# Kernel optimization log

Measured on AMD Instinct MI355X. Metric: run time of the kernel, lower is better.

## Reference

```python
import jax, jax.numpy as jnp
import numpy as np

B, S, D = 4, 2048, 1024
NEG = -1e9

def setup_inputs() -> dict:
    key = jax.random.key(0)
    ks = jax.random.split(key, 12)
    sc = 1.0 / np.sqrt(D)
    inp = {
        'query': jax.random.normal(ks[0], (B, S, D), jnp.float32),
        'key':   jax.random.normal(ks[1], (B, S, D), jnp.float32),
        'value': jax.random.normal(ks[2], (B, S, D), jnp.float32),
        'Wq': jax.random.normal(ks[3], (D, D), jnp.float32) * sc,
        'bq': jnp.zeros((D,), jnp.float32),
        'Wk': jax.random.normal(ks[4], (D, D), jnp.float32) * sc,
        'bk': jnp.zeros((D,), jnp.float32),
        'Wv': jax.random.normal(ks[5], (D, D), jnp.float32) * sc,
        'bv': jnp.zeros((D,), jnp.float32),
        'Wo': jax.random.normal(ks[6], (D, D), jnp.float32) * sc,
        'bo': jnp.zeros((D,), jnp.float32),
    }
    return inp

def reference(query, key, value, Wq, bq, Wk, bk, Wv, bv, Wo, bo):
    d_model = query.shape[-1]
    q = query @ Wq + bq            # [B,S,D]
    k = key   @ Wk + bk
    v = value @ Wv + bv
    # scores scaled by sqrt(d_model) (single head, full d_model)
    scores = jnp.einsum('bqd,bkd->bqk', q, k) / jnp.sqrt(jnp.float32(d_model))
    s = scores.shape[-1]
    causal = jnp.tril(jnp.ones((s, s), bool))  # True = keep
    scores = jnp.where(causal, scores, NEG)
    # log-softmax then exp for numerical stability (use_log_probs=True)
    attn = jnp.exp(jax.nn.log_softmax(scores, axis=-1))
    out = jnp.einsum('bqk,bkd->bqd', attn, v)
    return out @ Wo + bo
```

## Files before the change

kernel.cpp:

```cpp
#include <hip/hip_runtime.h>


typedef __attribute__((ext_vector_type(8))) short bf16x8_t;
typedef __attribute__((ext_vector_type(4))) float f32x4_t;

static __device__ __forceinline__ unsigned short f2b(float f) {
  union { float f; unsigned u; } c; c.f = f;
  unsigned u = c.u;
  u += 0x7fffu + ((u >> 16) & 1u);
  return (unsigned short)(u >> 16);
}

static __device__ __forceinline__ void gload16(const void* g, const void* l) {
  __builtin_amdgcn_global_load_lds(
      (const __attribute__((address_space(1))) void*)g,
      (__attribute__((address_space(3))) void*)(void*)(unsigned short*)l,
      16, 0, 0);
}

__global__ __launch_bounds__(256)
void prep_all(const float* __restrict__ q, const float* __restrict__ k,
              const float* __restrict__ v,
              unsigned short* __restrict__ qin, unsigned short* __restrict__ kin,
              unsigned short* __restrict__ vin,
              const float* __restrict__ wq, const float* __restrict__ wk,
              const float* __restrict__ wo, const float* __restrict__ wv,
              unsigned short* __restrict__ oq, unsigned short* __restrict__ ok,
              unsigned short* __restrict__ oo, unsigned short* __restrict__ ov)
{
  __shared__ unsigned short t[32][34];
  const int d = blockIdx.x;
  const int tid = threadIdx.x;
  if (d < 12288) {
    const int z = d >> 12;
    const int blk = d & 4095;
    const float* in = z == 0 ? q : (z == 1 ? k : v);
    unsigned short* out = z == 0 ? qin : (z == 1 ? kin : vin);
    const size_t base = ((size_t)blk * 256 + tid) * 8;
    const float4 x0 = *(const float4*)(in + base);
    const float4 x1 = *(const float4*)(in + base + 4);
    union { unsigned u[4]; uint4 v4; } pk;
    pk.u[0] = f2b(x0.x) | ((unsigned)f2b(x0.y) << 16);
    pk.u[1] = f2b(x0.z) | ((unsigned)f2b(x0.w) << 16);
    pk.u[2] = f2b(x1.x) | ((unsigned)f2b(x1.y) << 16);
    pk.u[3] = f2b(x1.z) | ((unsigned)f2b(x1.w) << 16);
    *(uint4*)(out + base) = pk.v4;
    return;
  }
  const int tt = d - 12288;
  const int z = tt >> 10;
  const int r = tt & 1023;
  const int by = r >> 5, bx = r & 31;
  const int x = tid & 31, y = tid >> 5;
  const float* in = z == 0 ? wq : (z == 1 ? wk : (z == 2 ? wo : wv));
  unsigned short* out = z == 0 ? oq : (z == 1 ? ok : (z == 2 ? oo : ov));
  if (z == 3) {
#pragma unroll
    for (int yy = y; yy < 32; yy += 8) {
      const int rr = by * 32 + yy, cc = bx * 32 + x;
      out[(size_t)rr * 1024 + cc] = f2b(in[(size_t)rr * 1024 + cc]);
    }
    return;
  }
#pragma unroll
  for (int yy = y; yy < 32; yy += 8)
    t[yy][x] = f2b(in[(size_t)(by * 32 + yy) * 1024 + bx * 32 + x]);
  __syncthreads();
#pragma unroll
  for (int yy = y; yy < 32; yy += 8)
    out[(size_t)(bx * 32 + yy) * 1024 + by * 32 + x] = t[x][yy];
}

template<bool OUT_BF16, int MODE>
static __device__ __forceinline__
void gemm_body(const unsigned short* __restrict__ Ab,
               const unsigned short* __restrict__ Bt,
               const float* __restrict__ bias, void* __restrict__ Cp,
               float* __restrict__ rowsum,
               int kEnd, int lda, int ldb, int ldc, float scale, int bx, int by)
{
  __shared__ unsigned short As[128 * 64];
  __shared__ unsigned short Bs[128 * 64];

  const int tid  = threadIdx.x;
  const int lane = tid & 63;
  const int wid  = tid >> 6;
  const int wr   = wid >> 1, wc = wid & 1;
  const int l15  = lane & 15, l4 = lane >> 4;

  const int srow_l = lane >> 3;
  const int schk   = lane & 7;

  f32x4_t acc[4][4];
#pragma unroll
  for (int m = 0; m < 4; ++m)
#pragma unroll
    for (int n = 0; n < 4; ++n) acc[m][n] = (f32x4_t){0.f, 0.f, 0.f, 0.f};

  for (int k0 = 0; k0 < kEnd; k0 += 64) {
#pragma unroll
    for (int i = 0; i < 4; ++i) {
      const int row = i * 32 + wid * 8 + srow_l;
      const size_t gr = (size_t)(by * 128 + row);
      const int g = schk ^ (row & 7);
      gload16(Ab + gr * lda + k0 + g * 8, &As[(i * 32 + wid * 8) * 64]);
    }
#pragma unroll
    for (int i = 0; i < 4; ++i) {
      const int row = i * 32 + wid * 8 + srow_l;
      const size_t gn = (size_t)(bx * 128 + row);
      const int g = schk ^ (row & 7);
      gload16(Bt + gn * ldb + k0 + g * 8, &Bs[(i * 32 + wid * 8) * 64]);
    }
    __syncthreads();

#pragma unroll
    for (int kk = 0; kk < 2; ++kk) {
      bf16x8_t a[4], b[4];
#pragma unroll
      for (int m = 0; m < 4; ++m) {
        const int row = wr * 64 + m * 16 + l15;
        const int c = (kk * 4 + l4) ^ (row & 7);
        a[m] = *(const bf16x8_t*)&As[row * 64 + c * 8];
      }
#pragma unroll
      for (int n = 0; n < 4; ++n) {
        const int row = wc * 64 + n * 16 + l15;
        const int c = (kk * 4 + l4) ^ (row & 7);
        b[n] = *(const bf16x8_t*)&Bs[row * 64 + c * 8];
      }
#pragma unroll
      for (int m = 0; m < 4; ++m)
#pragma unroll
        for (int n = 0; n < 4; ++n)
          acc[m][n] = __builtin_amdgcn_mfma_f32_16x16x32_bf16(a[m], b[n], acc[m][n], 0, 0, 0);
    }
    __syncthreads();
  }

  float*          Cf = (float*)Cp;
  unsigned short* Cb = (unsigned short*)Cp;
  if constexpr (MODE == 1) {
#pragma unroll
    for (int m = 0; m < 4; ++m)
#pragma unroll
      for (int j = 0; j < 4; ++j) {
        const int row = by * 128 + wr * 64 + m * 16 + l4 * 4 + j;
        float rsum = 0.f;
#pragma unroll
        for (int n = 0; n < 4; ++n) {
          const int col = bx * 128 + wc * 64 + n * 16 + l15;
          const float e = (col <= row) ? __expf(acc[m][n][j] * scale) : 0.f;
          Cb[(size_t)row * ldc + col] = f2b(e);
          rsum += e;
        }
#pragma unroll
        for (int off = 1; off < 16; off <<= 1) rsum += __shfl_xor(rsum, off);
        if (l15 == 0) atomicAdd(&rowsum[row], rsum);
      }
  } else if constexpr (MODE == 2) {
#pragma unroll
    for (int m = 0; m < 4; ++m)
#pragma unroll
      for (int n = 0; n < 4; ++n) {
        const int col = bx * 128 + wc * 64 + n * 16 + l15;
        const float bv = bias[col];
#pragma unroll
        for (int j = 0; j < 4; ++j) {
          const int row = by * 128 + wr * 64 + m * 16 + l4 * 4 + j;
          const float inv = 1.0f / rowsum[row];
          Cf[(size_t)row * ldc + col] = acc[m][n][j] * inv + bv;
        }
      }
  } else {
#pragma unroll
    for (int m = 0; m < 4; ++m)
#pragma unroll
      for (int n = 0; n < 4; ++n) {
        const int col = bx * 128 + wc * 64 + n * 16 + l15;
        const float bv = bias ? bias[col] : 0.f;
#pragma unroll
        for (int j = 0; j < 4; ++j) {
          const int row = by * 128 + wr * 64 + m * 16 + l4 * 4 + j;
          const float val = acc[m][n][j] * scale + bv;
          if (OUT_BF16) Cb[(size_t)row * ldc + col] = f2b(val);
          else          Cf[(size_t)row * ldc + col] = val;
        }
      }
  }
}

__global__ __launch_bounds__(256)
void wvo_bias2(const unsigned short* __restrict__ Wot,
               const unsigned short* __restrict__ Wvb,
               const float* __restrict__ bv, const float* __restrict__ Wo,
               const float* __restrict__ bo,
               unsigned short* __restrict__ WvoT_w, float* __restrict__ bias2)
{
  if (blockIdx.x < 64) {
    gemm_body<true, 0>(Wot, Wvb, nullptr, WvoT_w, nullptr,
                       1024, 1024, 1024, 1024, 1.f,
                       (int)blockIdx.x & 7, (int)blockIdx.x >> 3);
    return;
  }
  __shared__ float red[16][17];
  const int b = blockIdx.x - 64;
  const int ci = threadIdx.x & 15;
  const int rg = threadIdx.x >> 4;
  const int col = b * 16 + ci;
  float s = 0.f;
#pragma unroll 4
  for (int r = rg; r < 1024; r += 16)
    s += bv[r] * Wo[(size_t)r * 1024 + col];
  red[rg][ci] = s;
  __syncthreads();
  if (rg == 0) {
    float t = 0.f;
#pragma unroll
    for (int i = 0; i < 16; ++i) t += red[i][ci];
    bias2[col] = t + bo[col];
  }
}

__global__ __launch_bounds__(256)
void gemm_qkv3(const unsigned short* __restrict__ qin,
               const unsigned short* __restrict__ kin,
               const unsigned short* __restrict__ vin,
               const unsigned short* __restrict__ Wqt,
               const unsigned short* __restrict__ Wkt,
               const unsigned short* __restrict__ WvoT_w,
               const float* __restrict__ bq, const float* __restrict__ bk,
               unsigned short* __restrict__ qbuf, unsigned short* __restrict__ kbuf,
               unsigned short* __restrict__ vT)
{
  const int d = blockIdx.x;
  const int xcd = d & 7, j = d >> 3;
  const int G = xcd * 24 + (j >> 3);
  if (G < 64) {
    gemm_body<true, 0>(qin, Wqt, bq, qbuf, nullptr,
                       1024, 1024, 1024, 1024, 1.f, j & 7, G);
  } else if (G < 128) {
    gemm_body<true, 0>(kin, Wkt, bk, kbuf, nullptr,
                       1024, 1024, 1024, 1024, 1.f, j & 7, G - 64);
  } else {
    const int idx = (G - 128) * 8 + (j & 7);
    const int b  = idx >> 7;
    const int r  = idx & 127;
    const int by = r >> 4;
    const int bx = r & 15;
    gemm_body<true, 0>(WvoT_w, vin + (size_t)b * 2048 * 1024, nullptr,
                       vT + (size_t)b * 1024 * 2048, nullptr,
                       1024, 1024, 1024, 2048, 1.f, bx, by);
  }
}

__global__ __launch_bounds__(256)
void gemm_scores(const unsigned short* __restrict__ Q,
                 const unsigned short* __restrict__ Kb,
                 unsigned short* __restrict__ P, float* __restrict__ rowsum)
{
  const int d = blockIdx.x;
  const int t = (d & 7) * 68 + (d >> 3);
  const int bz = t / 136;
  const int tri = t - bz * 136;
  int by = (int)((sqrtf(8.f * tri + 1.f) - 1.f) * 0.5f);
  while ((by + 1) * (by + 2) / 2 <= tri) ++by;
  while (by * (by + 1) / 2 > tri) --by;
  const int bx = tri - by * (by + 1) / 2;
  gemm_body<true, 1>(Q + (size_t)bz * 2048 * 1024,
                     Kb + (size_t)bz * 2048 * 1024, nullptr,
                     P + (size_t)bz * 2048 * 2048,
                     rowsum + (size_t)bz * 2048,
                     1024, 1024, 1024, 2048, 0.03125f, bx, by);
}

__global__ __launch_bounds__(256)
void gemm_final(const unsigned short* __restrict__ P,
                const unsigned short* __restrict__ vT,
                const float* __restrict__ bias2, float* __restrict__ rowsum,
                float* __restrict__ out)
{
  const int d = blockIdx.x;
  const int xcd = d & 7, j = d >> 3;
  const int G = xcd * 8 + (j >> 3);
  const int bz = G >> 4;
  const int by = G & 15;
  const int bx = j & 7;
  const int kEnd = (by + 1) * 128;
  gemm_body<false, 2>(P + (size_t)bz * 2048 * 2048,
                      vT + (size_t)bz * 1024 * 2048, bias2,
                      out + (size_t)bz * 2048 * 1024,
                      rowsum + (size_t)bz * 2048,
                      kEnd, 2048, 2048, 1024, 1.f, bx, by);
}

extern "C" void kernel_launch(void* const* d_in, const int* in_sizes, int n_in,
                              void* d_out, int out_size, void* d_ws, size_t ws_size,
                              hipStream_t stream)
{
  const float* query = (const float*)d_in[0];
  const float* key   = (const float*)d_in[1];
  const float* value = (const float*)d_in[2];
  const float* Wq    = (const float*)d_in[3];
  const float* bq    = (const float*)d_in[4];
  const float* Wk    = (const float*)d_in[5];
  const float* bk    = (const float*)d_in[6];
  const float* Wv    = (const float*)d_in[7];
  const float* bv    = (const float*)d_in[8];
  const float* Wo    = (const float*)d_in[9];
  const float* bo    = (const float*)d_in[10];
  float* out = (float*)d_out;

  char* ws = (char*)d_ws;
  const size_t MB = 1024 * 1024;
  unsigned short* Wqt    = (unsigned short*)(ws + 0 * MB);
  unsigned short* Wkt    = (unsigned short*)(ws + 2 * MB);
  unsigned short* Wot    = (unsigned short*)(ws + 4 * MB);
  unsigned short* Wvb    = (unsigned short*)(ws + 6 * MB);
  unsigned short* WvoT_w = (unsigned short*)(ws + 8 * MB);
  float*          bias2  = (float*)(ws + 10 * MB);
  float*          rowsum = (float*)(ws + 11 * MB);
  unsigned short* qbuf   = (unsigned short*)(ws + 12 * MB);
  unsigned short* kbuf   = (unsigned short*)(ws + 28 * MB);
  unsigned short* vT     = (unsigned short*)(ws + 44 * MB);
  unsigned short* qin    = (unsigned short*)(ws + 60 * MB);
  unsigned short* kin    = (unsigned short*)(ws + 76 * MB);
  unsigned short* vin    = (unsigned short*)(ws + 92 * MB);
  unsigned short* Pbuf   = (unsigned short*)(ws + 108 * MB);

  hipMemsetAsync(rowsum, 0, 4 * 2048 * sizeof(float), stream);

  prep_all<<<16384, 256, 0, stream>>>(query, key, value, qin, kin, vin,
                                      Wq, Wk, Wo, Wv, Wqt, Wkt, Wot, Wvb);

  wvo_bias2<<<128, 256, 0, stream>>>(Wot, Wvb, bv, Wo, bo, WvoT_w, bias2);

  gemm_qkv3<<<1536, 256, 0, stream>>>(qin, kin, vin, Wqt, Wkt, WvoT_w,
                                      bq, bk, qbuf, kbuf, vT);

  gemm_scores<<<544, 256, 0, stream>>>(qbuf, kbuf, Pbuf, rowsum);

  gemm_final<<<512, 256, 0, stream>>>(Pbuf, vT, bias2, rowsum, out);
}
```

Measured before the change: 332.3 us.

## Regroup GEMM stages to merge Wvo product with QK projections and vT with scores

Fuses the small Wvo/bias2 kernel into the Q/K projection launch and moves the V projection (vT) into the scores launch, cutting one launch. Independent work now shares a grid, so the small tail of each stage overlaps with larger GEMMs. The final GEMM's block order changes so the longest causal row-blocks are scheduled first, spread across XCDs, which balances load. Shared memory is now declared per kernel and passed into gemm_body. The risk is extra per-block branching and different L2 locality from the new groupings.

```diff
diff --git a/kernel.cpp b/kernel.cpp
--- a/kernel.cpp
+++ b/kernel.cpp
@@ -73,15 +73,13 @@
 
 template<bool OUT_BF16, int MODE>
 static __device__ __forceinline__
-void gemm_body(const unsigned short* __restrict__ Ab,
+void gemm_body(unsigned short* __restrict__ As, unsigned short* __restrict__ Bs,
+               const unsigned short* __restrict__ Ab,
                const unsigned short* __restrict__ Bt,
                const float* __restrict__ bias, void* __restrict__ Cp,
                float* __restrict__ rowsum,
                int kEnd, int lda, int ldb, int ldc, float scale, int bx, int by)
 {
-  __shared__ unsigned short As[128 * 64];
-  __shared__ unsigned short Bs[128 * 64];
-
   const int tid  = threadIdx.x;
   const int lane = tid & 63;
   const int wid  = tid >> 6;
@@ -191,20 +189,44 @@
 }
 
 __global__ __launch_bounds__(256)
-void wvo_bias2(const unsigned short* __restrict__ Wot,
-               const unsigned short* __restrict__ Wvb,
-               const float* __restrict__ bv, const float* __restrict__ Wo,
-               const float* __restrict__ bo,
-               unsigned short* __restrict__ WvoT_w, float* __restrict__ bias2)
-{
-  if (blockIdx.x < 64) {
-    gemm_body<true, 0>(Wot, Wvb, nullptr, WvoT_w, nullptr,
-                       1024, 1024, 1024, 1024, 1.f,
-                       (int)blockIdx.x & 7, (int)blockIdx.x >> 3);
-    return;
-  }
-  __shared__ float red[16][17];
-  const int b = blockIdx.x - 64;
+void gemm_qk_wvo(const unsigned short* __restrict__ qin,
+                 const unsigned short* __restrict__ kin,
+                 const unsigned short* __restrict__ Wqt,
+                 const unsigned short* __restrict__ Wkt,
+                 const unsigned short* __restrict__ Wot,
+                 const unsigned short* __restrict__ Wvb,
+                 const float* __restrict__ bq, const float* __restrict__ bk,
+                 const float* __restrict__ bv, const float* __restrict__ Wo,
+                 const float* __restrict__ bo,
+                 unsigned short* __restrict__ qbuf,
+                 unsigned short* __restrict__ kbuf,
+                 unsigned short* __restrict__ WvoT_w,
+                 float* __restrict__ bias2)
+{
+  __shared__ unsigned short As[128 * 64];
+  __shared__ unsigned short Bs[128 * 64];
+  const int d = blockIdx.x;
+  if (d < 1024) {
+    const int xcd = d & 7, j = d >> 3;
+    const int G = xcd * 16 + (j >> 3);
+    const int z = G >> 6;
+    const int by = G & 63, bx = j & 7;
+    if (z == 0)
+      gemm_body<true, 0>(As, Bs, qin, Wqt, bq, qbuf, nullptr,
+                         1024, 1024, 1024, 1024, 1.f, bx, by);
+    else
+      gemm_body<true, 0>(As, Bs, kin, Wkt, bk, kbuf, nullptr,
+                         1024, 1024, 1024, 1024, 1.f, bx, by);
+    return;
+  }
+  if (d < 1088) {
+    const int w = d - 1024;
+    gemm_body<true, 0>(As, Bs, Wot, Wvb, nullptr, WvoT_w, nullptr,
+                       1024, 1024, 1024, 1024, 1.f, w & 7, w >> 3);
+    return;
+  }
+  float* red = (float*)As;
+  const int b = d - 1088;
   const int ci = threadIdx.x & 15;
   const int rg = threadIdx.x >> 4;
   const int col = b * 16 + ci;
@@ -212,66 +234,52 @@
 #pragma unroll 4
   for (int r = rg; r < 1024; r += 16)
     s += bv[r] * Wo[(size_t)r * 1024 + col];
-  red[rg][ci] = s;
+  red[rg * 17 + ci] = s;
   __syncthreads();
   if (rg == 0) {
     float t = 0.f;
 #pragma unroll
-    for (int i = 0; i < 16; ++i) t += red[i][ci];
+    for (int i = 0; i < 16; ++i) t += red[i * 17 + ci];
     bias2[col] = t + bo[col];
   }
 }
 
 __global__ __launch_bounds__(256)
-void gemm_qkv3(const unsigned short* __restrict__ qin,
-               const unsigned short* __restrict__ kin,
-               const unsigned short* __restrict__ vin,
-               const unsigned short* __restrict__ Wqt,
-               const unsigned short* __restrict__ Wkt,
-               const unsigned short* __restrict__ WvoT_w,
-               const float* __restrict__ bq, const float* __restrict__ bk,
-               unsigned short* __restrict__ qbuf, unsigned short* __restrict__ kbuf,
-               unsigned short* __restrict__ vT)
-{
+void gemm_scores_vt(const unsigned short* __restrict__ Q,
+                    const unsigned short* __restrict__ Kb,
+                    const unsigned short* __restrict__ vin,
+                    const unsigned short* __restrict__ WvoT_w,
+                    unsigned short* __restrict__ P, float* __restrict__ rowsum,
+                    unsigned short* __restrict__ vT)
+{
+  __shared__ unsigned short As[128 * 64];
+  __shared__ unsigned short Bs[128 * 64];
   const int d = blockIdx.x;
-  const int xcd = d & 7, j = d >> 3;
-  const int G = xcd * 24 + (j >> 3);
-  if (G < 64) {
-    gemm_body<true, 0>(qin, Wqt, bq, qbuf, nullptr,
-                       1024, 1024, 1024, 1024, 1.f, j & 7, G);
-  } else if (G < 128) {
-    gemm_body<true, 0>(kin, Wkt, bk, kbuf, nullptr,
-                       1024, 1024, 1024, 1024, 1.f, j & 7, G - 64);
-  } else {
-    const int idx = (G - 128) * 8 + (j & 7);
-    const int b  = idx >> 7;
-    const int r  = idx & 127;
-    const int by = r >> 4;
-    const int bx = r & 15;
-    gemm_body<true, 0>(WvoT_w, vin + (size_t)b * 2048 * 1024, nullptr,
-                       vT + (size_t)b * 1024 * 2048, nullptr,
-                       1024, 1024, 1024, 2048, 1.f, bx, by);
-  }
-}
-
-__global__ __launch_bounds__(256)
-void gemm_scores(const unsigned short* __restrict__ Q,
-                 const unsigned short* __restrict__ Kb,
-                 unsigned short* __restrict__ P, float* __restrict__ rowsum)
-{
-  const int d = blockIdx.x;
-  const int t = (d & 7) * 68 + (d >> 3);
-  const int bz = t / 136;
-  const int tri = t - bz * 136;
-  int by = (int)((sqrtf(8.f * tri + 1.f) - 1.f) * 0.5f);
-  while ((by + 1) * (by + 2) / 2 <= tri) ++by;
-  while (by * (by + 1) / 2 > tri) --by;
-  const int bx = tri - by * (by + 1) / 2;
-  gemm_body<true, 1>(Q + (size_t)bz * 2048 * 1024,
-                     Kb + (size_t)bz * 2048 * 1024, nullptr,
-                     P + (size_t)bz * 2048 * 2048,
-                     rowsum + (size_t)bz * 2048,
-                     1024, 1024, 1024, 2048, 0.03125f, bx, by);
+  if (d < 544) {
+    const int t = (d & 7) * 68 + (d >> 3);
+    const int bz = t / 136;
+    const int tri = t - bz * 136;
+    int by = (int)((sqrtf(8.f * tri + 1.f) - 1.f) * 0.5f);
+    while ((by + 1) * (by + 2) / 2 <= tri) ++by;
+    while (by * (by + 1) / 2 > tri) --by;
+    const int bx = tri - by * (by + 1) / 2;
+    gemm_body<true, 1>(As, Bs, Q + (size_t)bz * 2048 * 1024,
+                       Kb + (size_t)bz * 2048 * 1024, nullptr,
+                       P + (size_t)bz * 2048 * 2048,
+                       rowsum + (size_t)bz * 2048,
+                       1024, 1024, 1024, 2048, 0.03125f, bx, by);
+    return;
+  }
+  const int e = d - 544;
+  const int xcd = e & 7, j = e >> 3;
+  const int jj = (xcd * 8 + (j >> 3)) * 8 + (j & 7);
+  const int b  = jj >> 7;
+  const int r  = jj & 127;
+  const int by = r >> 4;
+  const int bx = r & 15;
+  gemm_body<true, 0>(As, Bs, WvoT_w, vin + (size_t)b * 2048 * 1024, nullptr,
+                     vT + (size_t)b * 1024 * 2048, nullptr,
+                     1024, 1024, 1024, 2048, 1.f, bx, by);
 }
 
 __global__ __launch_bounds__(256)
@@ -280,14 +288,16 @@
                 const float* __restrict__ bias2, float* __restrict__ rowsum,
                 float* __restrict__ out)
 {
+  __shared__ unsigned short As[128 * 64];
+  __shared__ unsigned short Bs[128 * 64];
   const int d = blockIdx.x;
   const int xcd = d & 7, j = d >> 3;
-  const int G = xcd * 8 + (j >> 3);
-  const int bz = G >> 4;
-  const int by = G & 15;
-  const int bx = j & 7;
+  const int s = j >> 3, bx = j & 7;
+  const int w = s * 8 + xcd;
+  const int by = (w < 32) ? (15 - (w >> 2)) : ((w - 32) >> 2);
+  const int bz = w & 3;
   const int kEnd = (by + 1) * 128;
-  gemm_body<false, 2>(P + (size_t)bz * 2048 * 2048,
+  gemm_body<false, 2>(As, Bs, P + (size_t)bz * 2048 * 2048,
                       vT + (size_t)bz * 1024 * 2048, bias2,
                       out + (size_t)bz * 2048 * 1024,
                       rowsum + (size_t)bz * 2048,
@@ -333,12 +343,12 @@
   prep_all<<<16384, 256, 0, stream>>>(query, key, value, qin, kin, vin,
                                       Wq, Wk, Wo, Wv, Wqt, Wkt, Wot, Wvb);
 
-  wvo_bias2<<<128, 256, 0, stream>>>(Wot, Wvb, bv, Wo, bo, WvoT_w, bias2);
-
-  gemm_qkv3<<<1536, 256, 0, stream>>>(qin, kin, vin, Wqt, Wkt, WvoT_w,
-                                      bq, bk, qbuf, kbuf, vT);
-
-  gemm_scores<<<544, 256, 0, stream>>>(qbuf, kbuf, Pbuf, rowsum);
+  gemm_qk_wvo<<<1152, 256, 0, stream>>>(qin, kin, Wqt, Wkt, Wot, Wvb,
+                                        bq, bk, bv, Wo, bo,
+                                        qbuf, kbuf, WvoT_w, bias2);
+
+  gemm_scores_vt<<<1056, 256, 0, stream>>>(qbuf, kbuf, vin, WvoT_w,
+                                           Pbuf, rowsum, vT);
 
   gemm_final<<<512, 256, 0, stream>>>(Pbuf, vT, bias2, rowsum, out);
 }
```

Measured after the change: 328.9 us. Within noise of the previous version (-1.0%).
